# Kernel tuning notes

Measured on AMD Instinct MI355X. Metric: run time of the kernel, lower is better.

Reference implementation:

```python
import jax, jax.numpy as jnp
import numpy as np

VOCAB = 100000
NUM_SENSES = 8
VEC_DIM = 128
BATCH = 16384
CTX = 10  # context words -> x has 2 + CTX columns


def setup_inputs() -> dict:
    key = jax.random.key(0)
    kx, kg, ks = jax.random.split(key, 3)
    x = jax.random.randint(kx, (BATCH, 2 + CTX), 0, VOCAB, dtype=jnp.int32)
    W_g = jax.random.normal(kg, (VOCAB, VEC_DIM), dtype=jnp.float32) * 0.1
    W_s = jax.random.normal(ks, (VOCAB, NUM_SENSES, VEC_DIM), dtype=jnp.float32) * 0.1
    return {"x": x, "W_g": W_g, "W_s": W_s}


def reference(x, W_g, W_s):
    # sum of global vectors of the context words: [B, D]
    sum_context = jnp.sum(W_g[x[:, 2:]], axis=1)
    # sense vectors of the target word: [B, K, D]
    sense_vecs = W_s[x[:, 0]]
    # per-sense score against the context: [B, K]
    scores = jnp.einsum("bkd,bd->bk", sense_vecs, sum_context)
    # route to best sense per example: [B]
    right_senses = jnp.argmax(scores, axis=1)
    # gather the chosen sense vector: [B, D]
    chosen = jnp.take_along_axis(sense_vecs, right_senses[:, None, None], axis=1)[:, 0, :]
    # dot with the global vector of the second word -> [B, 1], sigmoid activation
    dot_prod = jnp.einsum("bd,bd->b", chosen, W_g[x[:, 1]])[:, None]
    return jax.nn.sigmoid(dot_prod)
```

## Files before the change

kernel.cpp:

```cpp
#include <hip/hip_runtime.h>
#include <hip/hip_bf16.h>
#include <cmath>

#define BATCH     16384
#define CTX       10
#define NSENSE    8
#define VEC_DIM   128
#define XCOLS     (2 + CTX)

__global__ __launch_bounds__(256) void SenseEmbedding_40295383171457_kernel(
    const int*   __restrict__ x,
    const float* __restrict__ Wg,
    const float* __restrict__ Ws,
    float*       __restrict__ out)
{
    const int wave = (blockIdx.x * blockDim.x + threadIdx.x) >> 6;
    const int lane = threadIdx.x & 63;
    if (wave >= BATCH) return;

    const int* xr = x + wave * XCOLS;
    const int w0 = xr[0];
    const int w1 = xr[1];

    float2 csum = make_float2(0.f, 0.f);
    #pragma unroll
    for (int c = 0; c < CTX; ++c) {
        const int idx = xr[2 + c];
        const float2 g = *reinterpret_cast<const float2*>(
            Wg + (size_t)idx * VEC_DIM + 2 * lane);
        csum.x += g.x;
        csum.y += g.y;
    }

    const float* srow = Ws + (size_t)w0 * (NSENSE * VEC_DIM);
    float scores[NSENSE];
    #pragma unroll
    for (int k = 0; k < NSENSE; ++k) {
        const float2 s = *reinterpret_cast<const float2*>(
            srow + k * VEC_DIM + 2 * lane);
        float p = s.x * csum.x + s.y * csum.y;
        #pragma unroll
        for (int off = 32; off > 0; off >>= 1)
            p += __shfl_xor(p, off, 64);
        scores[k] = p;
    }

    int   best = 0;
    float bv   = scores[0];
    #pragma unroll
    for (int k = 1; k < NSENSE; ++k) {
        if (scores[k] > bv) { bv = scores[k]; best = k; }
    }

    const float2 ch = *reinterpret_cast<const float2*>(
        srow + best * VEC_DIM + 2 * lane);
    const float2 tg = *reinterpret_cast<const float2*>(
        Wg + (size_t)w1 * VEC_DIM + 2 * lane);
    float d = ch.x * tg.x + ch.y * tg.y;
    #pragma unroll
    for (int off = 32; off > 0; off >>= 1)
        d += __shfl_xor(d, off, 64);

    if (lane == 0) {
        out[wave] = 1.f / (1.f + expf(-d));
    }
}

extern "C" void kernel_launch(void* const* d_in, const int* in_sizes, int n_in,
                              void* d_out, int out_size, void* d_ws, size_t ws_size,
                              hipStream_t stream) {
    const int*   x  = (const int*)  d_in[0];
    const float* Wg = (const float*)d_in[1];
    const float* Ws = (const float*)d_in[2];
    float*       out = (float*)d_out;

    const int waves_per_block = 256 / 64;
    const int grid = (BATCH + waves_per_block - 1) / waves_per_block;
    SenseEmbedding_40295383171457_kernel<<<grid, 256, 0, stream>>>(x, Wg, Ws, out);
}
```

Baseline: 484.9 us.

## Map each batch element to 16 lanes with float4 loads instead of a full wave

Each batch element is now handled by a 16-lane group rather than a whole 64-lane wave. Every lane reads 8 floats per row through two float4 loads, and the shuffle reductions shrink from 6 steps to 4. The goal is fewer threads, wider memory transactions and shorter reductions for this gather-bound workload. In exchange the grid has a quarter as many blocks and each lane holds more registers.

```diff
diff --git a/kernel.cpp b/kernel.cpp
--- a/kernel.cpp
+++ b/kernel.cpp
@@ -14,34 +14,39 @@
     const float* __restrict__ Ws,
     float*       __restrict__ out)
 {
-    const int wave = (blockIdx.x * blockDim.x + threadIdx.x) >> 6;
-    const int lane = threadIdx.x & 63;
-    if (wave >= BATCH) return;
+    const int gtid = blockIdx.x * blockDim.x + threadIdx.x;
+    const int elem = gtid >> 4;
+    const int sub  = gtid & 15;
+    if (elem >= BATCH) return;
 
-    const int* xr = x + wave * XCOLS;
+    const int* xr = x + elem * XCOLS;
     const int w0 = xr[0];
     const int w1 = xr[1];
+    const int off = sub * 8;
 
-    float2 csum = make_float2(0.f, 0.f);
+    float4 c0 = make_float4(0.f, 0.f, 0.f, 0.f);
+    float4 c1 = make_float4(0.f, 0.f, 0.f, 0.f);
     #pragma unroll
     for (int c = 0; c < CTX; ++c) {
-        const int idx = xr[2 + c];
-        const float2 g = *reinterpret_cast<const float2*>(
-            Wg + (size_t)idx * VEC_DIM + 2 * lane);
-        csum.x += g.x;
-        csum.y += g.y;
+        const float* row = Wg + (size_t)xr[2 + c] * VEC_DIM + off;
+        const float4 a = *reinterpret_cast<const float4*>(row);
+        const float4 b = *reinterpret_cast<const float4*>(row + 4);
+        c0.x += a.x; c0.y += a.y; c0.z += a.z; c0.w += a.w;
+        c1.x += b.x; c1.y += b.y; c1.z += b.z; c1.w += b.w;
     }
 
     const float* srow = Ws + (size_t)w0 * (NSENSE * VEC_DIM);
     float scores[NSENSE];
     #pragma unroll
     for (int k = 0; k < NSENSE; ++k) {
-        const float2 s = *reinterpret_cast<const float2*>(
-            srow + k * VEC_DIM + 2 * lane);
-        float p = s.x * csum.x + s.y * csum.y;
+        const float* r = srow + k * VEC_DIM + off;
+        const float4 a = *reinterpret_cast<const float4*>(r);
+        const float4 b = *reinterpret_cast<const float4*>(r + 4);
+        float p = a.x * c0.x + a.y * c0.y + a.z * c0.z + a.w * c0.w
+                + b.x * c1.x + b.y * c1.y + b.z * c1.z + b.w * c1.w;
         #pragma unroll
-        for (int off = 32; off > 0; off >>= 1)
-            p += __shfl_xor(p, off, 64);
+        for (int s = 8; s > 0; s >>= 1)
+            p += __shfl_xor(p, s, 16);
         scores[k] = p;
     }
 
@@ -52,17 +57,20 @@
         if (scores[k] > bv) { bv = scores[k]; best = k; }
     }
 
-    const float2 ch = *reinterpret_cast<const float2*>(
-        srow + best * VEC_DIM + 2 * lane);
-    const float2 tg = *reinterpret_cast<const float2*>(
-        Wg + (size_t)w1 * VEC_DIM + 2 * lane);
-    float d = ch.x * tg.x + ch.y * tg.y;
+    const float* ch = srow + best * VEC_DIM + off;
+    const float4 ca = *reinterpret_cast<const float4*>(ch);
+    const float4 cb = *reinterpret_cast<const float4*>(ch + 4);
+    const float* tg = Wg + (size_t)w1 * VEC_DIM + off;
+    const float4 ta = *reinterpret_cast<const float4*>(tg);
+    const float4 tb = *reinterpret_cast<const float4*>(tg + 4);
+    float d = ca.x * ta.x + ca.y * ta.y + ca.z * ta.z + ca.w * ta.w
+            + cb.x * tb.x + cb.y * tb.y + cb.z * tb.z + cb.w * tb.w;
     #pragma unroll
-    for (int off = 32; off > 0; off >>= 1)
-        d += __shfl_xor(d, off, 64);
+    for (int s = 8; s > 0; s >>= 1)
+        d += __shfl_xor(d, s, 16);
 
-    if (lane == 0) {
-        out[wave] = 1.f / (1.f + expf(-d));
+    if (sub == 0) {
+        out[elem] = 1.f / (1.f + expf(-d));
     }
 }
 
@@ -74,7 +82,7 @@
     const float* Ws = (const float*)d_in[2];
     float*       out = (float*)d_out;
 
-    const int waves_per_block = 256 / 64;
-    const int grid = (BATCH + waves_per_block - 1) / waves_per_block;
+    const int elems_per_block = 256 / 16;
+    const int grid = (BATCH + elems_per_block - 1) / elems_per_block;
     SenseEmbedding_40295383171457_kernel<<<grid, 256, 0, stream>>>(x, Wg, Ws, out);
 }
```

Result: no change. 489.2 us (+0.9%).
